# Optimization experiments

Hardware: AMD Instinct MI355X
Metric: run time of the kernel (lower is better)

The kernel has to match this reference:

```python
import jax, jax.numpy as jnp
import numpy as np

RADIUS = 0.1
NSAMPLE = 32
EPS = 1e-5


def ball_query(radius, nsample, xyz):
    # xyz: [B, N, 3] -> idx [B, N, nsample] (query set == support set)
    B, N, _ = xyz.shape
    # pairwise squared distances [B, N, N]
    sq = jnp.sum((xyz[:, :, None, :] - xyz[:, None, :, :]) ** 2, axis=-1)
    grp = jnp.broadcast_to(jnp.arange(N, dtype=jnp.int32), (B, N, N))
    grp = jnp.where(sq > radius * radius, N, grp)
    grp = jnp.sort(grp, axis=-1)[:, :, :nsample]
    first = grp[:, :, 0:1]
    return jnp.where(grp == N, first, grp)  # self is always in-ball -> first valid


def index_points(points, idx):
    # points [B, N, C], idx [B, N, S] -> [B, N, S, C]
    B, N, S = idx.shape
    C = points.shape[-1]
    flat = jnp.take_along_axis(points, idx.reshape(B, N * S, 1), axis=1)
    return flat.reshape(B, N, S, C)


def bn(x, gamma, beta, mean, var, axis):
    # eval-mode batchnorm over channel axis
    shape = [1] * x.ndim
    shape[axis] = -1
    g = gamma.reshape(shape); b = beta.reshape(shape)
    m = mean.reshape(shape); v = var.reshape(shape)
    return (x - m) * (g * jax.lax.rsqrt(v + EPS)) + b


def setup_inputs() -> dict:
    key = jax.random.key(0)
    ks = jax.random.split(key, 8)
    B, N, C, E = 4, 4096, 128, 4
    H = C * E
    xyz = jax.random.uniform(ks[0], (B, N, 3), dtype=jnp.float32)
    feats = jax.random.normal(ks[1], (B, N, C), dtype=jnp.float32)
    s = 0.05
    Wn = jax.random.normal(ks[2], (C, C + 3), dtype=jnp.float32) * s
    W1 = jax.random.normal(ks[3], (H, C), dtype=jnp.float32) * s
    W2 = jax.random.normal(ks[4], (C, H), dtype=jnp.float32) * s
    def bnp(k, n):
        k1, k2 = jax.random.split(k)
        return (jnp.ones((n,), jnp.float32) + 0.01 * jax.random.normal(k1, (n,)),
                0.01 * jax.random.normal(k2, (n,)),
                jnp.zeros((n,), jnp.float32),
                jnp.ones((n,), jnp.float32))
    gn, bn_, mn, vn = bnp(ks[5], C)
    g1, b1, m1, v1 = bnp(ks[6], H)
    g2, b2, m2, v2 = bnp(ks[7], C)
    return dict(xyz=xyz, feats=feats, Wn=Wn, gn=gn, bn_=bn_, mn=mn, vn=vn,
                W1=W1, g1=g1, b1=b1, m1=m1, v1=v1,
                W2=W2, g2=g2, b2=b2, m2=m2, v2=v2)


def reference(xyz, feats, Wn, gn, bn_, mn, vn, W1, g1, b1, m1, v1, W2, g2, b2, m2, v2):
    B, N, C = feats.shape
    identity = feats  # [B, N, C]
    idx = ball_query(RADIUS, NSAMPLE, xyz)  # [B, N, S]
    grouped_xyz = index_points(xyz, idx) - xyz[:, :, None, :]  # [B, N, S, 3]
    grouped_xyz = grouped_xyz / RADIUS  # normalize_dp
    grouped_feats = index_points(feats, idx)  # [B, N, S, C]
    grouped = jnp.concatenate([grouped_xyz, grouped_feats], axis=-1)  # [B, N, S, C+3]
    # torch layout [B, C+3, S, N]; keep [B, N, S, C+3] and contract channels
    x = jnp.einsum('oc,bnsc->bnso', Wn, grouped)  # neighbor 1x1 conv
    x = jax.nn.relu(bn(x, gn, bn_, mn, vn, axis=3))
    x = jnp.max(x, axis=2)  # max over neighbors -> [B, N, C]
    # inverted bottleneck pointwise MLP
    h = jnp.einsum('hc,bnc->bnh', W1, x)
    h = jax.nn.relu(bn(h, g1, b1, m1, v1, axis=2))
    y = jnp.einsum('ch,bnh->bnc', W2, h)
    y = bn(y, g2, b2, m2, v2, axis=2)
    out = jax.nn.relu(y + identity)  # [B, N, C]
    return out
```

## Files before the change

### kernel.cpp

```cpp
#include <hip/hip_runtime.h>
#include <hip/hip_bf16.h>
#include <math.h>

static constexpr int BB = 4;
static constexpr int NN = 4096;
static constexpr int CC = 128;
static constexpr int HH = 512;
static constexpr int SS = 32;
static constexpr float EPSF = 1e-5f;
static constexpr int NCELL = 1000;

typedef __bf16 bf16_t;
typedef bf16_t bf16x8 __attribute__((ext_vector_type(8)));
typedef float f32x4 __attribute__((ext_vector_type(4)));

__device__ inline unsigned short f2bf(float f) {
    unsigned int u = __builtin_bit_cast(unsigned int, f);
    u += 0x7FFFu + ((u >> 16) & 1u);
    return (unsigned short)(u >> 16);
}
__device__ inline float bf2f(unsigned short s) {
    unsigned int u = ((unsigned int)s) << 16;
    return __builtin_bit_cast(float, u);
}
__device__ inline int cell_of(float v) {
    int c = (int)(v * 10.0f);
    return c > 9 ? 9 : (c < 0 ? 0 : c);
}

__device__ inline void gload_lds16(const void* g, void* l) {
    __builtin_amdgcn_global_load_lds(
        (const __attribute__((address_space(1))) unsigned int*)g,
        (__attribute__((address_space(3))) unsigned int*)l, 16, 0, 0);
}

__global__ __launch_bounds__(256)
void prep_kernel(const float* __restrict__ Wn, const float* __restrict__ W1,
                 const float* __restrict__ W2, const float* __restrict__ feats,
                 unsigned short* __restrict__ WnF, unsigned short* __restrict__ W1b,
                 unsigned short* __restrict__ W2b, unsigned short* __restrict__ featsb,
                 int* __restrict__ counts)
{
    const int blk = blockIdx.x;
    const int t   = threadIdx.x;
    if (blk < 576) {
        const int i = blk * 256 + t;
        if (i < 16384) {
            const int o = i >> 7, c = i & 127;
            WnF[i] = f2bf(Wn[o * 131 + 3 + c]);
        } else if (i < 16384 + 65536) {
            const int k = i - 16384;
            W1b[k] = f2bf(W1[k]);
        } else if (i < 16384 + 131072) {
            const int k = i - 16384 - 65536;
            W2b[k] = f2bf(W2[k]);
        }
    } else if (blk < 2624) {
        const int i = (blk - 576) * 256 + t;
        const float4 v = ((const float4*)feats)[i];
        unsigned long long pk = (unsigned long long)f2bf(v.x)
                              | ((unsigned long long)f2bf(v.y) << 16)
                              | ((unsigned long long)f2bf(v.z) << 32)
                              | ((unsigned long long)f2bf(v.w) << 48);
        ((unsigned long long*)featsb)[i] = pk;
    } else {
        const int i = (blk - 2624) * 256 + t;
        if (i < BB * NCELL) counts[i] = 0;
    }
}

__global__ __launch_bounds__(256)
void count_kernel(const float* __restrict__ xyz, int* __restrict__ counts)
{
    const int p = blockIdx.x * 256 + threadIdx.x;
    const int b = p >> 12;
    const float x = xyz[p * 3 + 0], y = xyz[p * 3 + 1], z = xyz[p * 3 + 2];
    const int cid = cell_of(z) * 100 + cell_of(y) * 10 + cell_of(x);
    atomicAdd(&counts[b * NCELL + cid], 1);
}

__global__ __launch_bounds__(1024)
void scan_kernel(const int* __restrict__ counts, int* __restrict__ starts,
                 int* __restrict__ cursor)
{
    const int t  = threadIdx.x;
    const int i0 = t * 4;
    int v[4];
    #pragma unroll
    for (int k = 0; k < 4; ++k)
        v[k] = (i0 + k < BB * NCELL) ? counts[i0 + k] : 0;
    const int s = v[0] + v[1] + v[2] + v[3];

    __shared__ int ls[1024];
    ls[t] = s;
    __syncthreads();
    #pragma unroll
    for (int off = 1; off < 1024; off <<= 1) {
        const int add = (t >= off) ? ls[t - off] : 0;
        __syncthreads();
        ls[t] += add;
        __syncthreads();
    }
    int ex = ls[t] - s;
    #pragma unroll
    for (int k = 0; k < 4; ++k) {
        if (i0 + k < BB * NCELL) {
            starts[i0 + k] = ex;
            cursor[i0 + k] = ex;
        }
        ex += v[k];
    }
    if (t == 1023) starts[BB * NCELL] = ls[1023];
}

__global__ __launch_bounds__(256)
void scatter_kernel(const float* __restrict__ xyz, int* __restrict__ cursor,
                    float4* __restrict__ spts)
{
    const int p = blockIdx.x * 256 + threadIdx.x;
    const int b = p >> 12;
    const int n = p & (NN - 1);
    const float x = xyz[p * 3 + 0], y = xyz[p * 3 + 1], z = xyz[p * 3 + 2];
    const int cid = cell_of(z) * 100 + cell_of(y) * 10 + cell_of(x);
    const int pos = atomicAdd(&cursor[b * NCELL + cid], 1);
    spts[pos] = make_float4(x, y, z, __int_as_float(n));
}

__global__ __launch_bounds__(64)
void ball_query_binned_kernel(const float* __restrict__ xyz,
                              const int* __restrict__ starts,
                              const float4* __restrict__ spts,
                              int* __restrict__ idx)
{
    const int p    = blockIdx.x;
    const int b    = p >> 12;
    const int lane = threadIdx.x;

    const float qx = xyz[p * 3 + 0];
    const float qy = xyz[p * 3 + 1];
    const float qz = xyz[p * 3 + 2];
    const int cx = cell_of(qx), cy = cell_of(qy), cz = cell_of(qz);
    const int xlo = cx > 0 ? cx - 1 : 0;
    const int xhi = cx < 9 ? cx + 1 : 9;

    __shared__ int list[128];
    __shared__ int res[SS];
    int cnt = 0;

    for (int dz = -1; dz <= 1; ++dz) {
        const int z2 = cz + dz;
        if (z2 < 0 || z2 > 9) continue;
        for (int dy = -1; dy <= 1; ++dy) {
            const int y2 = cy + dy;
            if (y2 < 0 || y2 > 9) continue;
            const int base = b * NCELL + z2 * 100 + y2 * 10;
            const int lo = starts[base + xlo];
            const int hi = starts[base + xhi + 1];
            for (int j0 = lo; j0 < hi; j0 += 64) {
                const int j = j0 + lane;
                bool in = false;
                int pi = 0;
                if (j < hi) {
                    const float4 s = spts[j];
                    float sq;
                    {
                        #pragma clang fp contract(off)
                        const float dx  = qx - s.x;
                        const float dyv = qy - s.y;
                        const float dzv = qz - s.z;
                        sq = dx * dx + dyv * dyv + dzv * dzv;
                    }
                    in = (sq <= 0.01f);
                    pi = __float_as_int(s.w);
                }
                const unsigned long long mask = __ballot(in);
                if (in) {
                    const int pos = cnt + __popcll(mask & ((1ull << lane) - 1ull));
                    if (pos < 128) list[pos] = pi;
                }
                cnt += (int)__popcll(mask);
            }
        }
    }
    __syncthreads();

    const int c = cnt < 128 ? cnt : 128;
    #pragma unroll
    for (int l0 = 0; l0 < 2; ++l0) {
        const int l = lane + l0 * 64;
        if (l < c) {
            const int v = list[l];
            int r = 0;
            for (int k = 0; k < c; ++k) r += (list[k] < v);
            if (r < SS) res[r] = v;
        }
    }
    __syncthreads();

    if (lane < SS) {
        const int m = c < SS ? c : SS;
        idx[(size_t)p * SS + lane] = (lane < m) ? res[lane] : res[0];
    }
}

__global__ __launch_bounds__(128)
void group_max_kernel(const float* __restrict__ xyz, const unsigned short* __restrict__ T,
                      const float* __restrict__ Wn,
                      const float* __restrict__ gn, const float* __restrict__ bnv,
                      const float* __restrict__ mn, const float* __restrict__ vn,
                      const int* __restrict__ idx, unsigned short* __restrict__ xout)
{
    const int p = blockIdx.x;
    const int b = p >> 12;
    const int o = threadIdx.x;

    __shared__ int   sj[SS];
    __shared__ float sgx[SS][3];

    const float* xb = xyz + (size_t)b * NN * 3;
    const float* q  = xyz + (size_t)p * 3;

    if (o < SS) {
        const int j = idx[(size_t)p * SS + o];
        sj[o] = j;
        sgx[o][0] = (xb[j * 3 + 0] - q[0]) / 0.1f;
        sgx[o][1] = (xb[j * 3 + 1] - q[1]) / 0.1f;
        sgx[o][2] = (xb[j * 3 + 2] - q[2]) / 0.1f;
    }
    __syncthreads();

    const float w0 = Wn[o * 131 + 0];
    const float w1 = Wn[o * 131 + 1];
    const float w2 = Wn[o * 131 + 2];
    const float sc = gn[o] / sqrtf(vn[o] + EPSF);
    const float sh = bnv[o] - mn[o] * sc;

    const unsigned short* Tb = T + (size_t)b * NN * CC;
    float mx = -INFINITY;
    #pragma unroll 8
    for (int s = 0; s < SS; ++s) {
        const float pre = bf2f(Tb[(size_t)sj[s] * CC + o])
                        + w0 * sgx[s][0] + w1 * sgx[s][1] + w2 * sgx[s][2];
        mx = fmaxf(mx, fmaf(sc, pre, sh));
    }
    xout[(size_t)p * CC + o] = f2bf(fmaxf(mx, 0.0f));
}

template<int MODE>
__global__ __launch_bounds__(256, 2)
void mfma_gemm_kernel(const unsigned short* __restrict__ A, const unsigned short* __restrict__ W,
                      const float* __restrict__ g, const float* __restrict__ bb,
                      const float* __restrict__ mu, const float* __restrict__ var,
                      const float* __restrict__ res, void* __restrict__ outv,
                      int M, int Nout, int K)
{
    constexpr int BM = 64, BN = 128, BK = 64;
    __shared__ char smem[(BM + BN) * BK * 2];
    char* sA = smem;
    char* sB = smem + BM * BK * 2;

    const int t    = threadIdx.x;
    const int lane = t & 63;
    const int w    = t >> 6;
    const int wm   = w >> 1;
    const int wn   = w & 1;
    const int m0   = blockIdx.x * BM;
    const int o0   = blockIdx.y * BN;
    const int Kb   = K * 2;

    f32x4 acc[2][4];
    #pragma unroll
    for (int i = 0; i < 2; ++i)
        #pragma unroll
        for (int j = 0; j < 4; ++j) acc[i][j] = f32x4{0.f, 0.f, 0.f, 0.f};

    const char* Ab = (const char*)A;
    const char* Wb = (const char*)W;

    for (int kc = 0; kc < K; kc += BK) {
        const int kcb = kc * 2;
        #pragma unroll
        for (int l = 0; l < 2; ++l) {
            const int q     = w * 2 + l;
            const int Lb    = q * 1024 + lane * 16;
            const int row   = Lb >> 7;
            const int inrow = Lb & 127;
            const char* src = Ab + (size_t)(m0 + row) * Kb + kcb + (inrow ^ ((row & 7) << 4));
            gload_lds16(src, sA + q * 1024);
        }
        #pragma unroll
        for (int l = 0; l < 4; ++l) {
            const int q     = w * 4 + l;
            const int Lb    = q * 1024 + lane * 16;
            const int row   = Lb >> 7;
            const int inrow = Lb & 127;
            const char* src = Wb + (size_t)(o0 + row) * Kb + kcb + (inrow ^ ((row & 7) << 4));
            gload_lds16(src, sB + q * 1024);
        }
        __syncthreads();

        #pragma unroll
        for (int ks = 0; ks < 2; ++ks) {
            const int kbyte = ks * 64 + (lane >> 4) * 16;
            bf16x8 af[2], bf[4];
            #pragma unroll
            for (int i = 0; i < 2; ++i) {
                const int r = wm * 32 + i * 16 + (lane & 15);
                af[i] = *(const bf16x8*)(sA + r * 128 + (kbyte ^ ((r & 7) << 4)));
            }
            #pragma unroll
            for (int j = 0; j < 4; ++j) {
                const int r = wn * 64 + j * 16 + (lane & 15);
                bf[j] = *(const bf16x8*)(sB + r * 128 + (kbyte ^ ((r & 7) << 4)));
            }
            #pragma unroll
            for (int i = 0; i < 2; ++i)
                #pragma unroll
                for (int j = 0; j < 4; ++j)
                    acc[i][j] = __builtin_amdgcn_mfma_f32_16x16x32_bf16(af[i], bf[j], acc[i][j], 0, 0, 0);
        }
        __syncthreads();
    }

    #pragma unroll
    for (int j = 0; j < 4; ++j) {
        const int col = o0 + wn * 64 + j * 16 + (lane & 15);
        float scg = 1.f, sh = 0.f, mm = 0.f;
        if constexpr (MODE >= 1) {
            scg = g[col] / sqrtf(var[col] + EPSF);
            mm  = mu[col];
            sh  = bb[col];
        }
        #pragma unroll
        for (int i = 0; i < 2; ++i) {
            const int rowb = m0 + wm * 32 + i * 16 + (lane >> 4) * 4;
            #pragma unroll
            for (int r = 0; r < 4; ++r) {
                float z = acc[i][j][r];
                if constexpr (MODE >= 1) z = (z - mm) * scg + sh;
                if constexpr (MODE == 2) z += res[(size_t)(rowb + r) * Nout + col];
                if constexpr (MODE >= 1) z = fmaxf(z, 0.f);
                if constexpr (MODE == 2)
                    ((float*)outv)[(size_t)(rowb + r) * Nout + col] = z;
                else
                    ((unsigned short*)outv)[(size_t)(rowb + r) * Nout + col] = f2bf(z);
            }
        }
    }
}

extern "C" void kernel_launch(void* const* d_in, const int* in_sizes, int n_in,
                              void* d_out, int out_size, void* d_ws, size_t ws_size,
                              hipStream_t stream)
{
    const float* xyz   = (const float*)d_in[0];
    const float* feats = (const float*)d_in[1];
    const float* Wn    = (const float*)d_in[2];
    const float* gn    = (const float*)d_in[3];
    const float* bn_   = (const float*)d_in[4];
    const float* mn    = (const float*)d_in[5];
    const float* vn    = (const float*)d_in[6];
    const float* W1    = (const float*)d_in[7];
    const float* g1    = (const float*)d_in[8];
    const float* b1    = (const float*)d_in[9];
    const float* m1    = (const float*)d_in[10];
    const float* v1    = (const float*)d_in[11];
    const float* W2    = (const float*)d_in[12];
    const float* g2    = (const float*)d_in[13];
    const float* b2    = (const float*)d_in[14];
    const float* m2    = (const float*)d_in[15];
    const float* v2    = (const float*)d_in[16];
    float* out = (float*)d_out;

    char* ws = (char*)d_ws;
    int*            idx    = (int*)(ws);
    int*            counts = (int*)(ws + 2097152);
    int*            starts = (int*)(ws + 2113536);
    int*            cursor = (int*)(ws + 2129920);
    float4*         spts   = (float4*)(ws + 2146304);
    unsigned short* WnF    = (unsigned short*)(ws +  2408448);
    unsigned short* W1b    = (unsigned short*)(ws +  2441216);
    unsigned short* W2b    = (unsigned short*)(ws +  2572288);
    unsigned short* featsb = (unsigned short*)(ws +  2703360);
    unsigned short* Tb     = (unsigned short*)(ws +  6897664);
    unsigned short* xb     = (unsigned short*)(ws + 11091968);
    unsigned short* hb     = (unsigned short*)(ws + 15286272);

    const int M = BB * NN;

    prep_kernel<<<2640, 256, 0, stream>>>(Wn, W1, W2, feats, WnF, W1b, W2b, featsb, counts);
    count_kernel<<<64, 256, 0, stream>>>(xyz, counts);
    scan_kernel<<<1, 1024, 0, stream>>>(counts, starts, cursor);
    scatter_kernel<<<64, 256, 0, stream>>>(xyz, cursor, spts);
    ball_query_binned_kernel<<<M, 64, 0, stream>>>(xyz, starts, spts, idx);

    mfma_gemm_kernel<0><<<dim3(M / 64, 1), 256, 0, stream>>>(
        featsb, WnF, nullptr, nullptr, nullptr, nullptr, nullptr, Tb, M, CC, CC);

    group_max_kernel<<<M, 128, 0, stream>>>(xyz, Tb, Wn, gn, bn_, mn, vn, idx, xb);

    mfma_gemm_kernel<1><<<dim3(M / 64, HH / 128), 256, 0, stream>>>(
        xb, W1b, g1, b1, m1, v1, nullptr, hb, M, HH, CC);

    mfma_gemm_kernel<2><<<dim3(M / 64, 1), 256, 0, stream>>>(
        hb, W2b, g2, b2, m2, v2, feats, out, M, CC, HH);
}
```

Before: 187.4 us.

## Fold neighbor BN into GEMM epilogue and vectorize grouped max kernel

Moves the neighbor batchnorm scale into a new GEMM epilogue mode. The scaled xyz weights and the BN shift are precomputed once in the prep kernel, so the gather/max loop does only three packed FMAs per element, and the shift and ReLU are applied after the max. The group_max kernel now handles 8 points per 256-thread block, with each thread covering 4 channels through 8-byte gathers and packed float2 math. This cuts block count, per-element arithmetic and scalar loads. Rounding now happens on the scaled T values in bf16, which changes precision slightly.

```diff
diff --git a/kernel.cpp b/kernel.cpp
--- a/kernel.cpp
+++ b/kernel.cpp
@@ -13,6 +13,7 @@
 typedef __bf16 bf16_t;
 typedef bf16_t bf16x8 __attribute__((ext_vector_type(8)));
 typedef float f32x4 __attribute__((ext_vector_type(4)));
+typedef float f32x2 __attribute__((ext_vector_type(2)));
 
 __device__ inline unsigned short f2bf(float f) {
     unsigned int u = __builtin_bit_cast(unsigned int, f);
@@ -23,9 +24,16 @@
     unsigned int u = ((unsigned int)s) << 16;
     return __builtin_bit_cast(float, u);
 }
+__device__ inline float u2f(unsigned int u) {
+    return __builtin_bit_cast(float, u);
+}
 __device__ inline int cell_of(float v) {
     int c = (int)(v * 10.0f);
     return c > 9 ? 9 : (c < 0 ? 0 : c);
+}
+__device__ inline f32x2 pk_fma_b(f32x2 a, float g, f32x2 c) {
+    const f32x2 gg = {g, g};
+    return a * gg + c;
 }
 
 __device__ inline void gload_lds16(const void* g, void* l) {
@@ -37,9 +45,11 @@
 __global__ __launch_bounds__(256)
 void prep_kernel(const float* __restrict__ Wn, const float* __restrict__ W1,
                  const float* __restrict__ W2, const float* __restrict__ feats,
+                 const float* __restrict__ gn, const float* __restrict__ bnv,
+                 const float* __restrict__ mn, const float* __restrict__ vn,
                  unsigned short* __restrict__ WnF, unsigned short* __restrict__ W1b,
                  unsigned short* __restrict__ W2b, unsigned short* __restrict__ featsb,
-                 int* __restrict__ counts)
+                 int* __restrict__ counts, float4* __restrict__ wfold)
 {
     const int blk = blockIdx.x;
     const int t   = threadIdx.x;
@@ -63,9 +73,15 @@
                               | ((unsigned long long)f2bf(v.z) << 32)
                               | ((unsigned long long)f2bf(v.w) << 48);
         ((unsigned long long*)featsb)[i] = pk;
-    } else {
+    } else if (blk < 2640) {
         const int i = (blk - 2624) * 256 + t;
         if (i < BB * NCELL) counts[i] = 0;
+    } else {
+        if (t < CC) {
+            const float sc = gn[t] / sqrtf(vn[t] + EPSF);
+            wfold[t] = make_float4(sc * Wn[t * 131 + 0], sc * Wn[t * 131 + 1],
+                                   sc * Wn[t * 131 + 2], bnv[t] - mn[t] * sc);
+        }
     }
 }
 
@@ -203,47 +219,61 @@
     }
 }
 
-__global__ __launch_bounds__(128)
-void group_max_kernel(const float* __restrict__ xyz, const unsigned short* __restrict__ T,
-                      const float* __restrict__ Wn,
-                      const float* __restrict__ gn, const float* __restrict__ bnv,
-                      const float* __restrict__ mn, const float* __restrict__ vn,
+__global__ __launch_bounds__(256)
+void group_max_kernel(const float* __restrict__ xyz,
+                      const unsigned short* __restrict__ T,
+                      const float4* __restrict__ wfold,
                       const int* __restrict__ idx, unsigned short* __restrict__ xout)
 {
-    const int p = blockIdx.x;
-    const int b = p >> 12;
-    const int o = threadIdx.x;
-
-    __shared__ int   sj[SS];
-    __shared__ float sgx[SS][3];
-
-    const float* xb = xyz + (size_t)b * NN * 3;
-    const float* q  = xyz + (size_t)p * 3;
-
-    if (o < SS) {
-        const int j = idx[(size_t)p * SS + o];
-        sj[o] = j;
-        sgx[o][0] = (xb[j * 3 + 0] - q[0]) / 0.1f;
-        sgx[o][1] = (xb[j * 3 + 1] - q[1]) / 0.1f;
-        sgx[o][2] = (xb[j * 3 + 2] - q[2]) / 0.1f;
+    const int t   = threadIdx.x;
+    const int ptl = t >> 5;
+    const int l   = t & 31;
+    const int p   = blockIdx.x * 8 + ptl;
+    const int b   = p >> 12;
+
+    __shared__ float4 sg[8][32];
+
+    {
+        const int j = idx[(size_t)p * SS + l];
+        const float* q  = xyz + (size_t)p * 3;
+        const float* pj = xyz + ((size_t)b * NN + j) * 3;
+        sg[ptl][l] = make_float4((pj[0] - q[0]) / 0.1f,
+                                 (pj[1] - q[1]) / 0.1f,
+                                 (pj[2] - q[2]) / 0.1f, __int_as_float(j));
     }
     __syncthreads();
 
-    const float w0 = Wn[o * 131 + 0];
-    const float w1 = Wn[o * 131 + 1];
-    const float w2 = Wn[o * 131 + 2];
-    const float sc = gn[o] / sqrtf(vn[o] + EPSF);
-    const float sh = bnv[o] - mn[o] * sc;
+    const int c0 = l * 4;
+    const float4 wa = wfold[c0 + 0], wb = wfold[c0 + 1];
+    const float4 wc = wfold[c0 + 2], wd = wfold[c0 + 3];
+    const f32x2 w0p0 = {wa.x, wb.x}, w1p0 = {wa.y, wb.y}, w2p0 = {wa.z, wb.z};
+    const f32x2 w0p1 = {wc.x, wd.x}, w1p1 = {wc.y, wd.y}, w2p1 = {wc.z, wd.z};
 
     const unsigned short* Tb = T + (size_t)b * NN * CC;
-    float mx = -INFINITY;
+    f32x2 mx0 = {-1e30f, -1e30f}, mx1 = {-1e30f, -1e30f};
+
     #pragma unroll 8
     for (int s = 0; s < SS; ++s) {
-        const float pre = bf2f(Tb[(size_t)sj[s] * CC + o])
-                        + w0 * sgx[s][0] + w1 * sgx[s][1] + w2 * sgx[s][2];
-        mx = fmaxf(mx, fmaf(sc, pre, sh));
-    }
-    xout[(size_t)p * CC + o] = f2bf(fmaxf(mx, 0.0f));
+        const float4 g = sg[ptl][s];
+        const int j = __float_as_int(g.w);
+        const uint2 tv = *(const uint2*)(Tb + (size_t)j * CC + c0);
+        f32x2 v0, v1;
+        v0.x = u2f(tv.x << 16); v0.y = u2f(tv.x & 0xFFFF0000u);
+        v1.x = u2f(tv.y << 16); v1.y = u2f(tv.y & 0xFFFF0000u);
+        v0 = pk_fma_b(w0p0, g.x, v0); v0 = pk_fma_b(w1p0, g.y, v0); v0 = pk_fma_b(w2p0, g.z, v0);
+        v1 = pk_fma_b(w0p1, g.x, v1); v1 = pk_fma_b(w1p1, g.y, v1); v1 = pk_fma_b(w2p1, g.z, v1);
+        mx0.x = fmaxf(mx0.x, v0.x); mx0.y = fmaxf(mx0.y, v0.y);
+        mx1.x = fmaxf(mx1.x, v1.x); mx1.y = fmaxf(mx1.y, v1.y);
+    }
+
+    const float r0 = fmaxf(mx0.x + wa.w, 0.f);
+    const float r1 = fmaxf(mx0.y + wb.w, 0.f);
+    const float r2 = fmaxf(mx1.x + wc.w, 0.f);
+    const float r3 = fmaxf(mx1.y + wd.w, 0.f);
+    uint2 o;
+    o.x = (unsigned)f2bf(r0) | ((unsigned)f2bf(r1) << 16);
+    o.y = (unsigned)f2bf(r2) | ((unsigned)f2bf(r3) << 16);
+    *(uint2*)(xout + (size_t)p * CC + c0) = o;
 }
 
 template<int MODE>
@@ -326,10 +356,13 @@
     for (int j = 0; j < 4; ++j) {
         const int col = o0 + wn * 64 + j * 16 + (lane & 15);
         float scg = 1.f, sh = 0.f, mm = 0.f;
-        if constexpr (MODE >= 1) {
+        if constexpr (MODE == 1 || MODE == 2) {
             scg = g[col] / sqrtf(var[col] + EPSF);
             mm  = mu[col];
             sh  = bb[col];
+        }
+        if constexpr (MODE == 3) {
+            scg = g[col] / sqrtf(var[col] + EPSF);
         }
         #pragma unroll
         for (int i = 0; i < 2; ++i) {
@@ -337,9 +370,10 @@
             #pragma unroll
             for (int r = 0; r < 4; ++r) {
                 float z = acc[i][j][r];
-                if constexpr (MODE >= 1) z = (z - mm) * scg + sh;
+                if constexpr (MODE == 1 || MODE == 2) z = (z - mm) * scg + sh;
+                if constexpr (MODE == 3) z = z * scg;
                 if constexpr (MODE == 2) z += res[(size_t)(rowb + r) * Nout + col];
-                if constexpr (MODE >= 1) z = fmaxf(z, 0.f);
+                if constexpr (MODE == 1 || MODE == 2) z = fmaxf(z, 0.f);
                 if constexpr (MODE == 2)
                     ((float*)outv)[(size_t)(rowb + r) * Nout + col] = z;
                 else
@@ -385,19 +419,21 @@
     unsigned short* Tb     = (unsigned short*)(ws +  6897664);
     unsigned short* xb     = (unsigned short*)(ws + 11091968);
     unsigned short* hb     = (unsigned short*)(ws + 15286272);
+    float4*         wfold  = (float4*)(ws + 32063488);
 
     const int M = BB * NN;
 
-    prep_kernel<<<2640, 256, 0, stream>>>(Wn, W1, W2, feats, WnF, W1b, W2b, featsb, counts);
+    prep_kernel<<<2641, 256, 0, stream>>>(Wn, W1, W2, feats, gn, bn_, mn, vn,
+                                          WnF, W1b, W2b, featsb, counts, wfold);
     count_kernel<<<64, 256, 0, stream>>>(xyz, counts);
     scan_kernel<<<1, 1024, 0, stream>>>(counts, starts, cursor);
     scatter_kernel<<<64, 256, 0, stream>>>(xyz, cursor, spts);
     ball_query_binned_kernel<<<M, 64, 0, stream>>>(xyz, starts, spts, idx);
 
-    mfma_gemm_kernel<0><<<dim3(M / 64, 1), 256, 0, stream>>>(
-        featsb, WnF, nullptr, nullptr, nullptr, nullptr, nullptr, Tb, M, CC, CC);
-
-    group_max_kernel<<<M, 128, 0, stream>>>(xyz, Tb, Wn, gn, bn_, mn, vn, idx, xb);
+    mfma_gemm_kernel<3><<<dim3(M / 64, 1), 256, 0, stream>>>(
+        featsb, WnF, gn, nullptr, nullptr, vn, nullptr, Tb, M, CC, CC);
+
+    group_max_kernel<<<M / 8, 256, 0, stream>>>(xyz, Tb, wfold, idx, xb);
 
     mfma_gemm_kernel<1><<<dim3(M / 64, HH / 128), 256, 0, stream>>>(
         xb, W1b, g1, b1, m1, v1, nullptr, hb, M, HH, CC);
```

Result: faster. 159.1 us (-15.1%).
